# Performance work log

Hardware: AMD Instinct MI355X
Metric: run time of the kernel (lower is better)

Reference implementation:

```python
import jax, jax.numpy as jnp
import numpy as np

D_MODEL = 512
NUM_HEADS = 8
DEPTH = D_MODEL // NUM_HEADS


def setup_inputs() -> dict:
    key = jax.random.key(0)
    ks = jax.random.split(key, 11)
    B, S = 2, 4096
    scale = 1.0 / np.sqrt(D_MODEL)
    inp = {
        "q": jax.random.normal(ks[0], (B, S, D_MODEL), jnp.float32),
        "k": jax.random.normal(ks[1], (B, S, D_MODEL), jnp.float32),
        "v": jax.random.normal(ks[2], (B, S, D_MODEL), jnp.float32),
        "wq_w": jax.random.normal(ks[3], (D_MODEL, D_MODEL), jnp.float32) * scale,
        "wq_b": jnp.zeros((D_MODEL,), jnp.float32),
        "wk_w": jax.random.normal(ks[4], (D_MODEL, D_MODEL), jnp.float32) * scale,
        "wk_b": jnp.zeros((D_MODEL,), jnp.float32),
        "wv_w": jax.random.normal(ks[5], (D_MODEL, D_MODEL), jnp.float32) * scale,
        "wv_b": jnp.zeros((D_MODEL,), jnp.float32),
        "wo_w": jax.random.normal(ks[6], (D_MODEL, D_MODEL), jnp.float32) * scale,
        "wo_b": jnp.zeros((D_MODEL,), jnp.float32),
    }
    return inp


def _split_heads(x):
    # [B, S, D] -> [B, H, S, depth]
    B, S, _ = x.shape
    return x.reshape(B, S, NUM_HEADS, DEPTH).transpose(0, 2, 1, 3)


def reference(q, k, v, wq_w, wq_b, wk_w, wk_b, wv_w, wv_b, wo_w, wo_b):
    B, S, _ = q.shape
    qh = _split_heads(q @ wq_w.T + wq_b)  # [B,H,S,d]
    kh = _split_heads(k @ wk_w.T + wk_b)
    vh = _split_heads(v @ wv_w.T + wv_b)
    logits = jnp.einsum('bhqd,bhkd->bhqk', qh, kh) / jnp.sqrt(
        jnp.asarray(DEPTH, jnp.float32))
    attn = jax.nn.softmax(logits, axis=-1)
    out = jnp.einsum('bhqk,bhkd->bhqd', attn, vh)  # [B,H,S,d]
    out = out.transpose(0, 2, 1, 3).reshape(B, S, D_MODEL)
    return out @ wo_w.T + wo_b
```

## Files before the change

### kernel.cpp

```cpp
#include <hip/hip_runtime.h>

typedef __attribute__((ext_vector_type(8))) short short8;
typedef __attribute__((ext_vector_type(4))) float float4v;

#define D_MODEL 512
#define NUM_HEADS 8
#define DEPTH 64
#define SEQ 4096
#define BATCH 2
#define MROWS (BATCH * SEQ)

#define SW(r, c) (((r) * 64) + ((((c) ^ ((r) & 7))) * 8))

static __device__ __forceinline__ unsigned short f2bf(float f) {
  unsigned int u = __builtin_bit_cast(unsigned int, f);
  u += 0x7FFFu + ((u >> 16) & 1u);
  return (unsigned short)(u >> 16);
}
static __device__ __forceinline__ unsigned int pk2(float a, float b) {
  return (unsigned int)f2bf(a) | ((unsigned int)f2bf(b) << 16);
}

struct CvtArgs {
  const float4v* src[7];
  uint2* dst[7];
  int n4[7];
};
__global__ __launch_bounds__(256) void cvt_all(CvtArgs a) {
  const int ti = blockIdx.y;
  const float4v* __restrict__ s = a.src[ti];
  uint2* __restrict__ d = a.dst[ti];
  const int n = a.n4[ti];
  for (int i = blockIdx.x * 256 + threadIdx.x; i < n; i += gridDim.x * 256) {
    float4v f = s[i];
    d[i] = make_uint2(pk2(f[0], f[1]), pk2(f[2], f[3]));
  }
}

template <int XFP32, int MODE>
__global__ __launch_bounds__(256) void gemm_bt(
    const void* __restrict__ Xv,
    const unsigned short* __restrict__ Wb,
    const float* __restrict__ bias,
    void* __restrict__ outv) {
  __shared__ unsigned short As[64 * 72];
  __shared__ unsigned short Bs[64 * 72];
  const int t = threadIdx.x;
  const int w = t >> 6, l = t & 63, lq = l >> 4, lm = l & 15;
  const int mBase = blockIdx.x * 64;
  const int nBase = blockIdx.y * 64;
  float4v acc[4] = {};
  for (int kc = 0; kc < D_MODEL; kc += 64) {
    __syncthreads();
#pragma unroll
    for (int p = 0; p < 2; ++p) {
      int idx = p * 256 + t;
      int r = idx >> 3, c = (idx & 7) * 8;
      if (XFP32) {
        const float* Xf = (const float*)Xv;
        float4v f0 = *reinterpret_cast<const float4v*>(&Xf[(size_t)(mBase + r) * D_MODEL + kc + c]);
        float4v f1 = *reinterpret_cast<const float4v*>(&Xf[(size_t)(mBase + r) * D_MODEL + kc + c + 4]);
        short8 s;
#pragma unroll
        for (int j = 0; j < 4; ++j) {
          s[j] = (short)f2bf(f0[j]);
          s[4 + j] = (short)f2bf(f1[j]);
        }
        *reinterpret_cast<short8*>(&As[r * 72 + c]) = s;
      } else {
        const unsigned short* Xb = (const unsigned short*)Xv;
        *reinterpret_cast<short8*>(&As[r * 72 + c]) =
            *reinterpret_cast<const short8*>(&Xb[(size_t)(mBase + r) * D_MODEL + kc + c]);
      }
      *reinterpret_cast<short8*>(&Bs[r * 72 + c]) =
          *reinterpret_cast<const short8*>(&Wb[(size_t)(nBase + r) * D_MODEL + kc + c]);
    }
    __syncthreads();
#pragma unroll
    for (int kk = 0; kk < 64; kk += 32) {
      short8 a = *reinterpret_cast<const short8*>(&As[(w * 16 + lm) * 72 + kk + lq * 8]);
#pragma unroll
      for (int f = 0; f < 4; ++f) {
        short8 b = *reinterpret_cast<const short8*>(&Bs[(f * 16 + lm) * 72 + kk + lq * 8]);
        acc[f] = __builtin_amdgcn_mfma_f32_16x16x32_bf16(a, b, acc[f], 0, 0, 0);
      }
    }
  }
  if (MODE == 1) {
    __syncthreads();
    unsigned short* T = As;
#pragma unroll
    for (int f = 0; f < 4; ++f) {
      int dl = f * 16 + lm;
      float bv = bias[nBase + dl];
      uint2 u;
      u.x = pk2(acc[f][0] + bv, acc[f][1] + bv);
      u.y = pk2(acc[f][2] + bv, acc[f][3] + bv);
      int chunk = 2 * w + (lq >> 1);
      *reinterpret_cast<uint2*>(&T[SW(dl, chunk) + (lq & 1) * 4]) = u;
    }
    __syncthreads();
    const int bb = mBase >> 12, s0v = mBase & 4095, h = nBase >> 6;
    const size_t vbase = ((size_t)(bb * NUM_HEADS + h)) * DEPTH * SEQ;
#pragma unroll
    for (int p = 0; p < 2; ++p) {
      int idx = p * 256 + t;
      int d = idx >> 3, c = idx & 7;
      *reinterpret_cast<short8*>(&((unsigned short*)outv)[vbase + (size_t)d * SEQ + s0v + c * 8]) =
          *reinterpret_cast<const short8*>(&T[SW(d, c)]);
    }
  } else {
#pragma unroll
    for (int f = 0; f < 4; ++f) {
      int gn = nBase + f * 16 + lm;
      float bv = bias[gn];
#pragma unroll
      for (int r = 0; r < 4; ++r) {
        int gm = mBase + w * 16 + lq * 4 + r;
        float v = acc[f][r] + bv;
        int bb = gm >> 12, s = gm & 4095;
        int h = gn >> 6, d = gn & 63;
        if (MODE == 0) {
          ((unsigned short*)outv)[(((size_t)(bb * NUM_HEADS + h) * SEQ + s) << 6) + d] = f2bf(v);
        } else {
          ((float*)outv)[(size_t)gm * D_MODEL + gn] = v;
        }
      }
    }
  }
}

__global__ __launch_bounds__(128) void attn(
    const unsigned short* __restrict__ Qh,
    const unsigned short* __restrict__ Kh,
    const unsigned short* __restrict__ Vt,
    unsigned short* __restrict__ AO)
{
  __shared__ unsigned short Ksub[2][64 * 64];
  __shared__ unsigned short Vsub[2][64 * 64];
  __shared__ unsigned short Psub[64 * 64];
  const int t = threadIdx.x;
  const int w = t >> 6;
  const int l = t & 63, lq = l >> 4, lm = l & 15;
  const int bh = blockIdx.y;
  const size_t base = (size_t)bh * SEQ * DEPTH;
  const int qbase = blockIdx.x * 64 + w * 32;
  const unsigned short* __restrict__ Kp = Kh + base;
  const unsigned short* __restrict__ Vp = Vt + base;

  short8 qf[2][2];
#pragma unroll
  for (int qb = 0; qb < 2; ++qb)
#pragma unroll
    for (int kk = 0; kk < 2; ++kk)
      qf[qb][kk] = *reinterpret_cast<const short8*>(
          &Qh[base + (size_t)(qbase + qb * 16 + lm) * DEPTH + kk * 32 + lq * 8]);

  float4v oacc[2][4] = {};
  float lsum[2] = {0.f, 0.f};
  short8 kreg[4], vreg[4];

#pragma unroll
  for (int p = 0; p < 4; ++p) {
    int idx = p * 128 + t;
    int r = idx >> 3, c = idx & 7;
    kreg[p] = *reinterpret_cast<const short8*>(&Kp[(size_t)r * DEPTH + c * 8]);
    vreg[p] = *reinterpret_cast<const short8*>(&Vp[(size_t)r * SEQ + c * 8]);
  }
#pragma unroll
  for (int p = 0; p < 4; ++p) {
    int idx = p * 128 + t;
    int r = idx >> 3, c = idx & 7;
    *reinterpret_cast<short8*>(&Ksub[0][SW(r, c)]) = kreg[p];
    *reinterpret_cast<short8*>(&Vsub[0][SW(r, c)]) = vreg[p];
  }
  __syncthreads();

  for (int it = 0; it < 64; ++it) {
    const int cur = it & 1;
    if (it < 63) {
      const int s0n = (it + 1) * 64;
#pragma unroll
      for (int p = 0; p < 4; ++p) {
        int idx = p * 128 + t;
        int r = idx >> 3, c = idx & 7;
        kreg[p] = *reinterpret_cast<const short8*>(&Kp[(size_t)(s0n + r) * DEPTH + c * 8]);
        vreg[p] = *reinterpret_cast<const short8*>(&Vp[(size_t)r * SEQ + s0n + c * 8]);
      }
    }
#pragma unroll
    for (int f = 0; f < 4; ++f) {
      float4v sacc[2] = {};
#pragma unroll
      for (int kk = 0; kk < 2; ++kk) {
        short8 a = *reinterpret_cast<const short8*>(&Ksub[cur][SW(f * 16 + lm, kk * 4 + lq)]);
        sacc[0] = __builtin_amdgcn_mfma_f32_16x16x32_bf16(a, qf[0][kk], sacc[0], 0, 0, 0);
        sacc[1] = __builtin_amdgcn_mfma_f32_16x16x32_bf16(a, qf[1][kk], sacc[1], 0, 0, 0);
      }
#pragma unroll
      for (int qb = 0; qb < 2; ++qb) {
        float p0 = __expf(sacc[qb][0] * 0.125f);
        float p1 = __expf(sacc[qb][1] * 0.125f);
        float p2 = __expf(sacc[qb][2] * 0.125f);
        float p3 = __expf(sacc[qb][3] * 0.125f);
        lsum[qb] += (p0 + p1) + (p2 + p3);
        uint2 u;
        u.x = pk2(p0, p1);
        u.y = pk2(p2, p3);
        int row = w * 32 + qb * 16 + lm;
        *reinterpret_cast<uint2*>(&Psub[SW(row, 2 * f + (lq >> 1)) + (lq & 1) * 4]) = u;
      }
    }
#pragma unroll
    for (int kk = 0; kk < 2; ++kk) {
      short8 a0 = *reinterpret_cast<const short8*>(&Psub[SW(w * 32 + lm, kk * 4 + lq)]);
      short8 a1 = *reinterpret_cast<const short8*>(&Psub[SW(w * 32 + 16 + lm, kk * 4 + lq)]);
#pragma unroll
      for (int df = 0; df < 4; ++df) {
        short8 b = *reinterpret_cast<const short8*>(&Vsub[cur][SW(df * 16 + lm, kk * 4 + lq)]);
        oacc[0][df] = __builtin_amdgcn_mfma_f32_16x16x32_bf16(a0, b, oacc[0][df], 0, 0, 0);
        oacc[1][df] = __builtin_amdgcn_mfma_f32_16x16x32_bf16(a1, b, oacc[1][df], 0, 0, 0);
      }
    }
    if (it < 63) {
#pragma unroll
      for (int p = 0; p < 4; ++p) {
        int idx = p * 128 + t;
        int r = idx >> 3, c = idx & 7;
        *reinterpret_cast<short8*>(&Ksub[cur ^ 1][SW(r, c)]) = kreg[p];
        *reinterpret_cast<short8*>(&Vsub[cur ^ 1][SW(r, c)]) = vreg[p];
      }
    }
    __syncthreads();
  }
  float rinv[2];
#pragma unroll
  for (int qb = 0; qb < 2; ++qb) {
    float v = lsum[qb];
    v += __shfl_xor(v, 16);
    v += __shfl_xor(v, 32);
    rinv[qb] = 1.0f / v;
  }
  const int bb = bh >> 3, h = bh & 7;
#pragma unroll
  for (int qb = 0; qb < 2; ++qb) {
#pragma unroll
    for (int r = 0; r < 4; ++r) {
      float rq = __shfl(rinv[qb], lq * 4 + r);
      int s = qbase + qb * 16 + lq * 4 + r;
#pragma unroll
      for (int df = 0; df < 4; ++df) {
        int d = df * 16 + lm;
        AO[((size_t)(bb * SEQ + s)) * D_MODEL + h * DEPTH + d] = f2bf(oacc[qb][df][r] * rq);
      }
    }
  }
}

extern "C" void kernel_launch(void* const* d_in, const int* in_sizes, int n_in,
                              void* d_out, int out_size, void* d_ws, size_t ws_size,
                              hipStream_t stream) {
  const void* q = d_in[0];
  const void* k = d_in[1];
  const void* v = d_in[2];
  const float* wq = (const float*)d_in[3];
  const float* bq = (const float*)d_in[4];
  const float* wk = (const float*)d_in[5];
  const float* bk = (const float*)d_in[6];
  const float* wv = (const float*)d_in[7];
  const float* bv = (const float*)d_in[8];
  const float* wo = (const float*)d_in[9];
  const float* bo = (const float*)d_in[10];

  const size_t HSD = (size_t)BATCH * NUM_HEADS * SEQ * DEPTH;
  const size_t WSZ = (size_t)D_MODEL * D_MODEL;
  unsigned short* ws = (unsigned short*)d_ws;
  unsigned short* Qh = ws;
  unsigned short* Kh = Qh + HSD;
  unsigned short* Vt = Kh + HSD;
  unsigned short* AO = Vt + HSD;
  unsigned short* Wc[4] = {AO + HSD, AO + HSD + WSZ, AO + HSD + 2 * WSZ, AO + HSD + 3 * WSZ};
  unsigned short* Xc[3] = {Wc[3] + WSZ, Wc[3] + WSZ + HSD, Wc[3] + WSZ + 2 * HSD};
  const bool full = ws_size >= (7 * HSD + 4 * WSZ) * 2;

  const float* wptr[4] = {wq, wk, wv, wo};
  CvtArgs ca = {};
  int ny;
  if (full) {
    const void* xin[3] = {q, k, v};
    for (int i = 0; i < 3; ++i) {
      ca.src[i] = (const float4v*)xin[i];
      ca.dst[i] = (uint2*)Xc[i];
      ca.n4[i] = (int)(HSD / 4);
    }
    for (int i = 0; i < 4; ++i) {
      ca.src[3 + i] = (const float4v*)wptr[i];
      ca.dst[3 + i] = (uint2*)Wc[i];
      ca.n4[3 + i] = (int)(WSZ / 4);
    }
    ny = 7;
  } else {
    for (int i = 0; i < 4; ++i) {
      ca.src[i] = (const float4v*)wptr[i];
      ca.dst[i] = (uint2*)Wc[i];
      ca.n4[i] = (int)(WSZ / 4);
    }
    ny = 4;
  }
  cvt_all<<<dim3(512, ny), 256, 0, stream>>>(ca);

  dim3 gGrid(MROWS / 64, D_MODEL / 64);
  if (full) {
    gemm_bt<0, 0><<<gGrid, 256, 0, stream>>>(Xc[0], Wc[0], bq, Qh);
    gemm_bt<0, 0><<<gGrid, 256, 0, stream>>>(Xc[1], Wc[1], bk, Kh);
    gemm_bt<0, 1><<<gGrid, 256, 0, stream>>>(Xc[2], Wc[2], bv, Vt);
  } else {
    gemm_bt<1, 0><<<gGrid, 256, 0, stream>>>(q, Wc[0], bq, Qh);
    gemm_bt<1, 0><<<gGrid, 256, 0, stream>>>(k, Wc[1], bk, Kh);
    gemm_bt<1, 1><<<gGrid, 256, 0, stream>>>(v, Wc[2], bv, Vt);
  }
  attn<<<dim3(SEQ / 64, BATCH * NUM_HEADS), 128, 0, stream>>>(Qh, Kh, Vt, AO);
  gemm_bt<0, 2><<<gGrid, 256, 0, stream>>>(AO, Wc[3], bo, d_out);
}
```

Baseline: 283.8 us.

## Batch QKV GEMMs in one launch, fold softmax scale into Q, widen attention blocks

The three Q/K/V projection GEMMs now run as a single launch over a z-dimension of the grid. The softmax scale times log2(e) is folded into the Q projection epilogue so the attention kernel can use exp2f with no per-element multiply. The attention kernel goes from 128 to 256 threads per block with 16 query rows per wave instead of 32. This halves each wave's register footprint and MFMA work but doubles the number of waves sharing each K/V tile. A workspace-tier fallback that converts weights to bf16 inside the GEMM is also added.

```diff
diff --git a/kernel.cpp b/kernel.cpp
--- a/kernel.cpp
+++ b/kernel.cpp
@@ -9,6 +9,7 @@
 #define SEQ 4096
 #define BATCH 2
 #define MROWS (BATCH * SEQ)
+#define SCALE_Q 0.18033688011112043f
 
 #define SW(r, c) (((r) * 64) + ((((c) ^ ((r) & 7))) * 8))
 
@@ -37,14 +38,21 @@
   }
 }
 
-template <int XFP32, int MODE>
-__global__ __launch_bounds__(256) void gemm_bt(
-    const void* __restrict__ Xv,
-    const unsigned short* __restrict__ Wb,
-    const float* __restrict__ bias,
-    void* __restrict__ outv) {
+struct QkvArgs {
+  const void* X[3];
+  const void* W[3];
+  const float* bias[3];
+  unsigned short* out[3];
+};
+template <int XFP32, int WFP32>
+__global__ __launch_bounds__(256) void gemm_qkv(QkvArgs a) {
   __shared__ unsigned short As[64 * 72];
   __shared__ unsigned short Bs[64 * 72];
+  const int z = blockIdx.z;
+  const void* __restrict__ Xv = a.X[z];
+  const void* __restrict__ Wv = a.W[z];
+  const float* __restrict__ bias = a.bias[z];
+  unsigned short* __restrict__ outv = a.out[z];
   const int t = threadIdx.x;
   const int w = t >> 6, l = t & 63, lq = l >> 4, lm = l & 15;
   const int mBase = blockIdx.x * 64;
@@ -72,21 +80,35 @@
         *reinterpret_cast<short8*>(&As[r * 72 + c]) =
             *reinterpret_cast<const short8*>(&Xb[(size_t)(mBase + r) * D_MODEL + kc + c]);
       }
-      *reinterpret_cast<short8*>(&Bs[r * 72 + c]) =
-          *reinterpret_cast<const short8*>(&Wb[(size_t)(nBase + r) * D_MODEL + kc + c]);
+      if (WFP32) {
+        const float* Wf = (const float*)Wv;
+        float4v f0 = *reinterpret_cast<const float4v*>(&Wf[(size_t)(nBase + r) * D_MODEL + kc + c]);
+        float4v f1 = *reinterpret_cast<const float4v*>(&Wf[(size_t)(nBase + r) * D_MODEL + kc + c + 4]);
+        short8 s;
+#pragma unroll
+        for (int j = 0; j < 4; ++j) {
+          s[j] = (short)f2bf(f0[j]);
+          s[4 + j] = (short)f2bf(f1[j]);
+        }
+        *reinterpret_cast<short8*>(&Bs[r * 72 + c]) = s;
+      } else {
+        const unsigned short* Wb = (const unsigned short*)Wv;
+        *reinterpret_cast<short8*>(&Bs[r * 72 + c]) =
+            *reinterpret_cast<const short8*>(&Wb[(size_t)(nBase + r) * D_MODEL + kc + c]);
+      }
     }
     __syncthreads();
 #pragma unroll
     for (int kk = 0; kk < 64; kk += 32) {
-      short8 a = *reinterpret_cast<const short8*>(&As[(w * 16 + lm) * 72 + kk + lq * 8]);
+      short8 av = *reinterpret_cast<const short8*>(&As[(w * 16 + lm) * 72 + kk + lq * 8]);
 #pragma unroll
       for (int f = 0; f < 4; ++f) {
         short8 b = *reinterpret_cast<const short8*>(&Bs[(f * 16 + lm) * 72 + kk + lq * 8]);
-        acc[f] = __builtin_amdgcn_mfma_f32_16x16x32_bf16(a, b, acc[f], 0, 0, 0);
-      }
-    }
-  }
-  if (MODE == 1) {
+        acc[f] = __builtin_amdgcn_mfma_f32_16x16x32_bf16(av, b, acc[f], 0, 0, 0);
+      }
+    }
+  }
+  if (z == 2) {
     __syncthreads();
     unsigned short* T = As;
 #pragma unroll
@@ -106,10 +128,11 @@
     for (int p = 0; p < 2; ++p) {
       int idx = p * 256 + t;
       int d = idx >> 3, c = idx & 7;
-      *reinterpret_cast<short8*>(&((unsigned short*)outv)[vbase + (size_t)d * SEQ + s0v + c * 8]) =
+      *reinterpret_cast<short8*>(&outv[vbase + (size_t)d * SEQ + s0v + c * 8]) =
           *reinterpret_cast<const short8*>(&T[SW(d, c)]);
     }
   } else {
+    const float scale = (z == 0) ? SCALE_Q : 1.0f;
 #pragma unroll
     for (int f = 0; f < 4; ++f) {
       int gn = nBase + f * 16 + lm;
@@ -117,20 +140,77 @@
 #pragma unroll
       for (int r = 0; r < 4; ++r) {
         int gm = mBase + w * 16 + lq * 4 + r;
-        float v = acc[f][r] + bv;
+        float v = (acc[f][r] + bv) * scale;
         int bb = gm >> 12, s = gm & 4095;
         int h = gn >> 6, d = gn & 63;
-        if (MODE == 0) {
-          ((unsigned short*)outv)[(((size_t)(bb * NUM_HEADS + h) * SEQ + s) << 6) + d] = f2bf(v);
-        } else {
-          ((float*)outv)[(size_t)gm * D_MODEL + gn] = v;
+        outv[(((size_t)(bb * NUM_HEADS + h) * SEQ + s) << 6) + d] = f2bf(v);
+      }
+    }
+  }
+}
+
+template <int WFP32>
+__global__ __launch_bounds__(256) void gemm_out(
+    const unsigned short* __restrict__ Xb,
+    const void* __restrict__ Wv,
+    const float* __restrict__ bias,
+    float* __restrict__ out) {
+  __shared__ unsigned short As[64 * 72];
+  __shared__ unsigned short Bs[64 * 72];
+  const int t = threadIdx.x;
+  const int w = t >> 6, l = t & 63, lq = l >> 4, lm = l & 15;
+  const int mBase = blockIdx.x * 64;
+  const int nBase = blockIdx.y * 64;
+  float4v acc[4] = {};
+  for (int kc = 0; kc < D_MODEL; kc += 64) {
+    __syncthreads();
+#pragma unroll
+    for (int p = 0; p < 2; ++p) {
+      int idx = p * 256 + t;
+      int r = idx >> 3, c = (idx & 7) * 8;
+      *reinterpret_cast<short8*>(&As[r * 72 + c]) =
+          *reinterpret_cast<const short8*>(&Xb[(size_t)(mBase + r) * D_MODEL + kc + c]);
+      if (WFP32) {
+        const float* Wf = (const float*)Wv;
+        float4v f0 = *reinterpret_cast<const float4v*>(&Wf[(size_t)(nBase + r) * D_MODEL + kc + c]);
+        float4v f1 = *reinterpret_cast<const float4v*>(&Wf[(size_t)(nBase + r) * D_MODEL + kc + c + 4]);
+        short8 s;
+#pragma unroll
+        for (int j = 0; j < 4; ++j) {
+          s[j] = (short)f2bf(f0[j]);
+          s[4 + j] = (short)f2bf(f1[j]);
         }
-      }
-    }
-  }
-}
-
-__global__ __launch_bounds__(128) void attn(
+        *reinterpret_cast<short8*>(&Bs[r * 72 + c]) = s;
+      } else {
+        const unsigned short* Wb = (const unsigned short*)Wv;
+        *reinterpret_cast<short8*>(&Bs[r * 72 + c]) =
+            *reinterpret_cast<const short8*>(&Wb[(size_t)(nBase + r) * D_MODEL + kc + c]);
+      }
+    }
+    __syncthreads();
+#pragma unroll
+    for (int kk = 0; kk < 64; kk += 32) {
+      short8 av = *reinterpret_cast<const short8*>(&As[(w * 16 + lm) * 72 + kk + lq * 8]);
+#pragma unroll
+      for (int f = 0; f < 4; ++f) {
+        short8 b = *reinterpret_cast<const short8*>(&Bs[(f * 16 + lm) * 72 + kk + lq * 8]);
+        acc[f] = __builtin_amdgcn_mfma_f32_16x16x32_bf16(av, b, acc[f], 0, 0, 0);
+      }
+    }
+  }
+#pragma unroll
+  for (int f = 0; f < 4; ++f) {
+    int gn = nBase + f * 16 + lm;
+    float bv = bias[gn];
+#pragma unroll
+    for (int r = 0; r < 4; ++r) {
+      int gm = mBase + w * 16 + lq * 4 + r;
+      out[(size_t)gm * D_MODEL + gn] = acc[f][r] + bv;
+    }
+  }
+}
+
+__global__ __launch_bounds__(256) void attn(
     const unsigned short* __restrict__ Qh,
     const unsigned short* __restrict__ Kh,
     const unsigned short* __restrict__ Vt,
@@ -144,32 +224,30 @@
   const int l = t & 63, lq = l >> 4, lm = l & 15;
   const int bh = blockIdx.y;
   const size_t base = (size_t)bh * SEQ * DEPTH;
-  const int qbase = blockIdx.x * 64 + w * 32;
+  const int qbase = blockIdx.x * 64 + w * 16;
   const unsigned short* __restrict__ Kp = Kh + base;
   const unsigned short* __restrict__ Vp = Vt + base;
 
-  short8 qf[2][2];
-#pragma unroll
-  for (int qb = 0; qb < 2; ++qb)
-#pragma unroll
-    for (int kk = 0; kk < 2; ++kk)
-      qf[qb][kk] = *reinterpret_cast<const short8*>(
-          &Qh[base + (size_t)(qbase + qb * 16 + lm) * DEPTH + kk * 32 + lq * 8]);
-
-  float4v oacc[2][4] = {};
-  float lsum[2] = {0.f, 0.f};
-  short8 kreg[4], vreg[4];
-
-#pragma unroll
-  for (int p = 0; p < 4; ++p) {
-    int idx = p * 128 + t;
+  short8 qf[2];
+#pragma unroll
+  for (int kk = 0; kk < 2; ++kk)
+    qf[kk] = *reinterpret_cast<const short8*>(
+        &Qh[base + (size_t)(qbase + lm) * DEPTH + kk * 32 + lq * 8]);
+
+  float4v oacc[4] = {};
+  float lsum = 0.f;
+  short8 kreg[2], vreg[2];
+
+#pragma unroll
+  for (int p = 0; p < 2; ++p) {
+    int idx = p * 256 + t;
     int r = idx >> 3, c = idx & 7;
     kreg[p] = *reinterpret_cast<const short8*>(&Kp[(size_t)r * DEPTH + c * 8]);
     vreg[p] = *reinterpret_cast<const short8*>(&Vp[(size_t)r * SEQ + c * 8]);
   }
 #pragma unroll
-  for (int p = 0; p < 4; ++p) {
-    int idx = p * 128 + t;
+  for (int p = 0; p < 2; ++p) {
+    int idx = p * 256 + t;
     int r = idx >> 3, c = idx & 7;
     *reinterpret_cast<short8*>(&Ksub[0][SW(r, c)]) = kreg[p];
     *reinterpret_cast<short8*>(&Vsub[0][SW(r, c)]) = vreg[p];
@@ -181,8 +259,8 @@
     if (it < 63) {
       const int s0n = (it + 1) * 64;
 #pragma unroll
-      for (int p = 0; p < 4; ++p) {
-        int idx = p * 128 + t;
+      for (int p = 0; p < 2; ++p) {
+        int idx = p * 256 + t;
         int r = idx >> 3, c = idx & 7;
         kreg[p] = *reinterpret_cast<const short8*>(&Kp[(size_t)(s0n + r) * DEPTH + c * 8]);
         vreg[p] = *reinterpret_cast<const short8*>(&Vp[(size_t)r * SEQ + s0n + c * 8]);
@@ -190,42 +268,35 @@
     }
 #pragma unroll
     for (int f = 0; f < 4; ++f) {
-      float4v sacc[2] = {};
+      float4v sacc = {};
 #pragma unroll
       for (int kk = 0; kk < 2; ++kk) {
         short8 a = *reinterpret_cast<const short8*>(&Ksub[cur][SW(f * 16 + lm, kk * 4 + lq)]);
-        sacc[0] = __builtin_amdgcn_mfma_f32_16x16x32_bf16(a, qf[0][kk], sacc[0], 0, 0, 0);
-        sacc[1] = __builtin_amdgcn_mfma_f32_16x16x32_bf16(a, qf[1][kk], sacc[1], 0, 0, 0);
-      }
-#pragma unroll
-      for (int qb = 0; qb < 2; ++qb) {
-        float p0 = __expf(sacc[qb][0] * 0.125f);
-        float p1 = __expf(sacc[qb][1] * 0.125f);
-        float p2 = __expf(sacc[qb][2] * 0.125f);
-        float p3 = __expf(sacc[qb][3] * 0.125f);
-        lsum[qb] += (p0 + p1) + (p2 + p3);
-        uint2 u;
-        u.x = pk2(p0, p1);
-        u.y = pk2(p2, p3);
-        int row = w * 32 + qb * 16 + lm;
-        *reinterpret_cast<uint2*>(&Psub[SW(row, 2 * f + (lq >> 1)) + (lq & 1) * 4]) = u;
-      }
+        sacc = __builtin_amdgcn_mfma_f32_16x16x32_bf16(a, qf[kk], sacc, 0, 0, 0);
+      }
+      float p0 = exp2f(sacc[0]);
+      float p1 = exp2f(sacc[1]);
+      float p2 = exp2f(sacc[2]);
+      float p3 = exp2f(sacc[3]);
+      lsum += (p0 + p1) + (p2 + p3);
+      uint2 u;
+      u.x = pk2(p0, p1);
+      u.y = pk2(p2, p3);
+      *reinterpret_cast<uint2*>(&Psub[SW(w * 16 + lm, 2 * f + (lq >> 1)) + (lq & 1) * 4]) = u;
     }
 #pragma unroll
     for (int kk = 0; kk < 2; ++kk) {
-      short8 a0 = *reinterpret_cast<const short8*>(&Psub[SW(w * 32 + lm, kk * 4 + lq)]);
-      short8 a1 = *reinterpret_cast<const short8*>(&Psub[SW(w * 32 + 16 + lm, kk * 4 + lq)]);
+      short8 a = *reinterpret_cast<const short8*>(&Psub[SW(w * 16 + lm, kk * 4 + lq)]);
 #pragma unroll
       for (int df = 0; df < 4; ++df) {
         short8 b = *reinterpret_cast<const short8*>(&Vsub[cur][SW(df * 16 + lm, kk * 4 + lq)]);
-        oacc[0][df] = __builtin_amdgcn_mfma_f32_16x16x32_bf16(a0, b, oacc[0][df], 0, 0, 0);
-        oacc[1][df] = __builtin_amdgcn_mfma_f32_16x16x32_bf16(a1, b, oacc[1][df], 0, 0, 0);
+        oacc[df] = __builtin_amdgcn_mfma_f32_16x16x32_bf16(a, b, oacc[df], 0, 0, 0);
       }
     }
     if (it < 63) {
 #pragma unroll
-      for (int p = 0; p < 4; ++p) {
-        int idx = p * 128 + t;
+      for (int p = 0; p < 2; ++p) {
+        int idx = p * 256 + t;
         int r = idx >> 3, c = idx & 7;
         *reinterpret_cast<short8*>(&Ksub[cur ^ 1][SW(r, c)]) = kreg[p];
         *reinterpret_cast<short8*>(&Vsub[cur ^ 1][SW(r, c)]) = vreg[p];
@@ -233,26 +304,19 @@
     }
     __syncthreads();
   }
-  float rinv[2];
-#pragma unroll
-  for (int qb = 0; qb < 2; ++qb) {
-    float v = lsum[qb];
-    v += __shfl_xor(v, 16);
-    v += __shfl_xor(v, 32);
-    rinv[qb] = 1.0f / v;
-  }
+  float v = lsum;
+  v += __shfl_xor(v, 16);
+  v += __shfl_xor(v, 32);
+  float rinv = 1.0f / v;
   const int bb = bh >> 3, h = bh & 7;
 #pragma unroll
-  for (int qb = 0; qb < 2; ++qb) {
-#pragma unroll
-    for (int r = 0; r < 4; ++r) {
-      float rq = __shfl(rinv[qb], lq * 4 + r);
-      int s = qbase + qb * 16 + lq * 4 + r;
-#pragma unroll
-      for (int df = 0; df < 4; ++df) {
-        int d = df * 16 + lm;
-        AO[((size_t)(bb * SEQ + s)) * D_MODEL + h * DEPTH + d] = f2bf(oacc[qb][df][r] * rq);
-      }
+  for (int r = 0; r < 4; ++r) {
+    float rq = __shfl(rinv, lq * 4 + r);
+    int s = qbase + lq * 4 + r;
+#pragma unroll
+    for (int df = 0; df < 4; ++df) {
+      int d = df * 16 + lm;
+      AO[((size_t)(bb * SEQ + s)) * D_MODEL + h * DEPTH + d] = f2bf(oacc[df][r] * rq);
     }
   }
 }
@@ -281,44 +345,50 @@
   unsigned short* AO = Vt + HSD;
   unsigned short* Wc[4] = {AO + HSD, AO + HSD + WSZ, AO + HSD + 2 * WSZ, AO + HSD + 3 * WSZ};
   unsigned short* Xc[3] = {Wc[3] + WSZ, Wc[3] + WSZ + HSD, Wc[3] + WSZ + 2 * HSD};
-  const bool full = ws_size >= (7 * HSD + 4 * WSZ) * 2;
+  const int tier = (ws_size >= (7 * HSD + 4 * WSZ) * 2) ? 1
+                 : (ws_size >= (4 * HSD + 4 * WSZ) * 2) ? 2 : 3;
 
   const float* wptr[4] = {wq, wk, wv, wo};
-  CvtArgs ca = {};
-  int ny;
-  if (full) {
-    const void* xin[3] = {q, k, v};
-    for (int i = 0; i < 3; ++i) {
-      ca.src[i] = (const float4v*)xin[i];
-      ca.dst[i] = (uint2*)Xc[i];
-      ca.n4[i] = (int)(HSD / 4);
+  const void* xin[3] = {q, k, v};
+
+  if (tier < 3) {
+    CvtArgs ca = {};
+    int ny = 0;
+    if (tier == 1) {
+      for (int i = 0; i < 3; ++i) {
+        ca.src[ny] = (const float4v*)xin[i];
+        ca.dst[ny] = (uint2*)Xc[i];
+        ca.n4[ny++] = (int)(HSD / 4);
+      }
     }
     for (int i = 0; i < 4; ++i) {
-      ca.src[3 + i] = (const float4v*)wptr[i];
-      ca.dst[3 + i] = (uint2*)Wc[i];
-      ca.n4[3 + i] = (int)(WSZ / 4);
-    }
-    ny = 7;
+      ca.src[ny] = (const float4v*)wptr[i];
+      ca.dst[ny] = (uint2*)Wc[i];
+      ca.n4[ny++] = (int)(WSZ / 4);
+    }
+    cvt_all<<<dim3(512, ny), 256, 0, stream>>>(ca);
+  }
+
+  QkvArgs qa;
+  qa.bias[0] = bq; qa.bias[1] = bk; qa.bias[2] = bv;
+  qa.out[0] = Qh; qa.out[1] = Kh; qa.out[2] = Vt;
+  dim3 gGrid(MROWS / 64, D_MODEL / 64, 3);
+  if (tier == 1) {
+    for (int i = 0; i < 3; ++i) { qa.X[i] = Xc[i]; qa.W[i] = Wc[i]; }
+    gemm_qkv<0, 0><<<gGrid, 256, 0, stream>>>(qa);
+  } else if (tier == 2) {
+    for (int i = 0; i < 3; ++i) { qa.X[i] = xin[i]; qa.W[i] = Wc[i]; }
+    gemm_qkv<1, 0><<<gGrid, 256, 0, stream>>>(qa);
   } else {
-    for (int i = 0; i < 4; ++i) {
-      ca.src[i] = (const float4v*)wptr[i];
-      ca.dst[i] = (uint2*)Wc[i];
-      ca.n4[i] = (int)(WSZ / 4);
-    }
-    ny = 4;
-  }
-  cvt_all<<<dim3(512, ny), 256, 0, stream>>>(ca);
-
-  dim3 gGrid(MROWS / 64, D_MODEL / 64);
-  if (full) {
-    gemm_bt<0, 0><<<gGrid, 256, 0, stream>>>(Xc[0], Wc[0], bq, Qh);
-    gemm_bt<0, 0><<<gGrid, 256, 0, stream>>>(Xc[1], Wc[1], bk, Kh);
-    gemm_bt<0, 1><<<gGrid, 256, 0, stream>>>(Xc[2], Wc[2], bv, Vt);
-  } else {
-    gemm_bt<1, 0><<<gGrid, 256, 0, stream>>>(q, Wc[0], bq, Qh);
-    gemm_bt<1, 0><<<gGrid, 256, 0, stream>>>(k, Wc[1], bk, Kh);
-    gemm_bt<1, 1><<<gGrid, 256, 0, stream>>>(v, Wc[2], bv, Vt);
-  }
-  attn<<<dim3(SEQ / 64, BATCH * NUM_HEADS), 128, 0, stream>>>(Qh, Kh, Vt, AO);
-  gemm_bt<0, 2><<<gGrid, 256, 0, stream>>>(AO, Wc[3], bo, d_out);
-}
+    for (int i = 0; i < 3; ++i) { qa.X[i] = xin[i]; qa.W[i] = wptr[i]; }
+    gemm_qkv<1, 1><<<gGrid, 256, 0, stream>>>(qa);
+  }
+
+  attn<<<dim3(SEQ / 64, BATCH * NUM_HEADS), 256, 0, stream>>>(Qh, Kh, Vt, AO);
+
+  dim3 oGrid(MROWS / 64, D_MODEL / 64);
+  if (tier < 3)
+    gemm_out<0><<<oGrid, 256, 0, stream>>>(AO, Wc[3], bo, (float*)d_out);
+  else
+    gemm_out<1><<<oGrid, 256, 0, stream>>>(AO, wo, bo, (float*)d_out);
+}
```

New measurement: 287.9 us. No clear change (+1.4%).
